# Performance work log

Hardware: AMD Instinct MI355X
Metric: run time of the kernel (lower is better)

Reference implementation:

```python
import jax, jax.numpy as jnp
import numpy as np

N_NODES = 100000
N_EDGES = 3200000
N_GRAPHS = 1024


def gcn_conv(x, src, dst, W, b):
    """GCNConv with symmetric normalization and implicit self-loops.
    x: [N, Fin], src/dst: [E] int, W: [Fin, Fout], b: [Fout]."""
    n = x.shape[0]
    h = x @ W  # [N, Fout]
    # degree including self-loop
    deg = jnp.zeros((n,), h.dtype).at[dst].add(1.0) + 1.0
    dinv = deg ** -0.5
    norm = dinv[src] * dinv[dst]  # [E]
    agg = jnp.zeros_like(h).at[dst].add(norm[:, None] * h[src])
    # self-loop contribution: dinv[i]^2 * h[i]
    agg = agg + (dinv * dinv)[:, None] * h
    return agg + b


def setup_inputs() -> dict:
    key = jax.random.key(0)
    ks = jax.random.split(key, 12)
    F, H = 128, 64
    x = jax.random.normal(ks[0], (N_NODES, F), jnp.float32)
    edge_index = jax.random.randint(ks[1], (2, N_EDGES), 0, N_NODES, jnp.int32)
    batch = jnp.sort(jax.random.randint(ks[2], (N_NODES,), 0, N_GRAPHS, jnp.int32))
    def w(k, i, o):
        return jax.random.normal(k, (i, o), jnp.float32) * (1.0 / np.sqrt(i))
    return {
        "x": x, "edge_index": edge_index, "batch": batch,
        "W1": w(ks[3], F, H), "b1": jnp.zeros((H,), jnp.float32),
        "W2": w(ks[4], H, H), "b2": jnp.zeros((H,), jnp.float32),
        "W3": w(ks[5], H, H // 2), "b3": jnp.zeros((H // 2,), jnp.float32),
        "Wc1": w(ks[6], H // 2, H // 4), "bc1": jnp.zeros((H // 4,), jnp.float32),
        "Wc2": w(ks[7], H // 4, 16), "bc2": jnp.zeros((16,), jnp.float32),
    }


def reference(x, edge_index, batch, W1, b1, W2, b2, W3, b3, Wc1, bc1, Wc2, bc2):
    src, dst = edge_index[0], edge_index[1]
    h = jax.nn.relu(gcn_conv(x, src, dst, W1, b1))
    h = jax.nn.relu(gcn_conv(h, src, dst, W2, b2))
    h = jax.nn.relu(gcn_conv(h, src, dst, W3, b3))
    # global mean pool over graphs (dropout is identity at inference)
    sums = jax.ops.segment_sum(h, batch, num_segments=N_GRAPHS)
    counts = jax.ops.segment_sum(jnp.ones((h.shape[0],), h.dtype), batch,
                                 num_segments=N_GRAPHS)
    pooled = sums / jnp.maximum(counts, 1.0)[:, None]  # [G, 32]
    z = jax.nn.relu(pooled @ Wc1 + bc1)
    logits = z @ Wc2 + bc2
    return jax.nn.log_softmax(logits, axis=-1)
```

## Files before the change

### kernel.cpp

```cpp
#include <hip/hip_runtime.h>
#include <hip/hip_bf16.h>
#include <hip/hip_fp16.h>
#include <math.h>


constexpr int BSHIFT = 8;
constexpr int BMASK  = 255;
constexpr int BCAP   = 10240;
constexpr int EPB    = 4096;

__global__ __launch_bounds__(512) void partition_kernel(const int* __restrict__ src,
    const int* __restrict__ dst, int* __restrict__ bucket_cnt,
    unsigned* __restrict__ part, unsigned* __restrict__ runmap,
    int E, int nbuckets, int nblk) {
  __shared__ int lcnt[512];
  __shared__ int lscan[512];
  __shared__ int lcur[512];
  __shared__ unsigned spay[EPB];
  const int t = threadIdx.x;
  const int blk = blockIdx.x;
  const int base = blk * EPB;
  const int lim = min(EPB, E - base);
  int s[8], d[8];
#pragma unroll
  for (int j = 0; j < 8; ++j) {
    int idx = base + j * 512 + t;
    if (idx < E) { s[j] = src[idx]; d[j] = dst[idx]; } else d[j] = -1;
  }
  lcnt[t] = 0;
  __syncthreads();
#pragma unroll
  for (int j = 0; j < 8; ++j)
    if (d[j] >= 0) atomicAdd(&lcnt[d[j] >> BSHIFT], 1);
  __syncthreads();
  const int myv = lcnt[t];
  lscan[t] = myv;
  __syncthreads();
  for (int dd = 1; dd < 512; dd <<= 1) {
    int v = 0;
    if (t >= dd) v = lscan[t - dd];
    __syncthreads();
    if (t >= dd) lscan[t] += v;
    __syncthreads();
  }
  const int excl = lscan[t] - myv;
  if (t < nbuckets) {
    runmap[(size_t)t * nblk + blk] = (unsigned)excl | ((unsigned)myv << 16);
    if (myv > 0) atomicAdd(&bucket_cnt[t], myv);
  }
  lcur[t] = excl;
  __syncthreads();
#pragma unroll
  for (int j = 0; j < 8; ++j) {
    if (d[j] >= 0) {
      int b = d[j] >> BSHIFT;
      int pos = atomicAdd(&lcur[b], 1);
      spay[pos] = ((unsigned)(d[j] & BMASK) << 17) | (unsigned)s[j];
    }
  }
  __syncthreads();
#pragma unroll
  for (int j = 0; j < 8; ++j) {
    int i = j * 512 + t;
    if (i < lim) part[base + i] = spay[i];
  }
}

__global__ __launch_bounds__(256) void scan_buckets_kernel(const int* __restrict__ cnt,
    int* __restrict__ base, int nb) {
  __shared__ int sh[512];
  const int t = threadIdx.x;
  sh[t] = (t < nb) ? cnt[t] : 0;
  sh[t + 256] = (t + 256 < nb) ? cnt[t + 256] : 0;
  __syncthreads();
  for (int d = 1; d < 512; d <<= 1) {
    int v0 = 0, v1 = 0;
    if (t >= d) v0 = sh[t - d];
    if (t + 256 >= d) v1 = sh[t + 256 - d];
    __syncthreads();
    if (t >= d) sh[t] += v0;
    if (t + 256 >= d) sh[t + 256] += v1;
    __syncthreads();
  }
  if (t < nb) base[t] = (t == 0) ? 0 : sh[t - 1];
  if (t + 256 < nb) base[t + 256] = sh[t + 255];
}

__global__ __launch_bounds__(512) void fill_bucket_kernel(
    const unsigned* __restrict__ part, const unsigned* __restrict__ runmap,
    const int* __restrict__ bucket_cnt, const int* __restrict__ bucket_base,
    int* __restrict__ offs, float* __restrict__ dinv, int* __restrict__ csr,
    int N, int E, int nblk) {
  __shared__ unsigned ebuf[BCAP];
  __shared__ int rsh[1024];
  __shared__ int ldeg[256];
  __shared__ int lscan[512];
  const int b = blockIdx.x;
  const int t = threadIdx.x;
  const int nb0 = b << BSHIFT;
  const int nn = min(1 << BSHIFT, N - nb0);
  const int wbase = bucket_base[b];
  const int cnt = min(bucket_cnt[b], BCAP);
  const unsigned r0 = (t < nblk) ? runmap[(size_t)b * nblk + t] : 0u;
  const unsigned r1 = (t + 512 < nblk) ? runmap[(size_t)b * nblk + t + 512] : 0u;
  const int c0 = (int)(r0 >> 16), c1 = (int)(r1 >> 16);
  rsh[t] = c0; rsh[t + 512] = c1;
  if (t < 256) ldeg[t] = 0;
  __syncthreads();
  for (int dd = 1; dd < 1024; dd <<= 1) {
    int x0 = 0, x1 = 0;
    if (t >= dd) x0 = rsh[t - dd];
    x1 = rsh[t + 512 - dd];
    __syncthreads();
    if (t >= dd) rsh[t] += x0;
    rsh[t + 512] += x1;
    __syncthreads();
  }
  {
    int rb = rsh[t] - c0;
    if (c0 > 0) {
      const unsigned* p = part + (size_t)t * EPB + (r0 & 0xFFFFu);
      for (int k = 0; k < c0; ++k) { int o = rb + k; if (o < BCAP) ebuf[o] = p[k]; }
    }
    int rb1 = rsh[t + 512] - c1;
    if (c1 > 0) {
      const unsigned* p = part + (size_t)(t + 512) * EPB + (r1 & 0xFFFFu);
      for (int k = 0; k < c1; ++k) { int o = rb1 + k; if (o < BCAP) ebuf[o] = p[k]; }
    }
  }
  __syncthreads();
  for (int i = t; i < cnt; i += 512) atomicAdd(&ldeg[ebuf[i] >> 17], 1);
  __syncthreads();
  const int myv = (t < 256) ? ldeg[t] : 0;
  lscan[t] = myv;
  __syncthreads();
  for (int d = 1; d < 256; d <<= 1) {
    int v = 0;
    if (t >= d && t < 256) v = lscan[t - d];
    __syncthreads();
    if (t >= d && t < 256) lscan[t] += v;
    __syncthreads();
  }
  const int excl = lscan[t] - myv;
  if (t < nn) {
    offs[nb0 + t] = wbase + excl;
    dinv[nb0 + t] = rsqrtf((float)(myv + 1));
  }
  if (t == 0 && nb0 + nn == N) offs[N] = E;
  if (t < 256) ldeg[t] = excl;
  __syncthreads();
  for (int i = t; i < cnt; i += 512) {
    unsigned v = ebuf[i];
    int pos = atomicAdd(&ldeg[v >> 17], 1);
    if (pos < BCAP) csr[wbase + pos] = (int)(v & 0x1FFFF);
  }
}

template <int K, int M>
__global__ __launch_bounds__(256) void gemm_kernel(const float* __restrict__ X,
    const float* __restrict__ W, __half* __restrict__ Y, int n) {
  constexpr int RPB = 32;
  constexpr int XST = K + 4;
  constexpr int MC = M / 16;
  __shared__ __align__(16) float Ws[K * M];
  __shared__ __align__(16) float Xs[RPB * XST];
  const int tid = threadIdx.x;
  const int row0 = blockIdx.x * RPB;
  for (int i = tid * 4; i < K * M; i += 1024)
    *reinterpret_cast<float4*>(&Ws[i]) = *reinterpret_cast<const float4*>(&W[i]);
  for (int i = tid * 4; i < RPB * K; i += 1024) {
    int r = i / K, k = i - r * K;
    int gr = row0 + r;
    float4 v = make_float4(0.f, 0.f, 0.f, 0.f);
    if (gr < n) v = *reinterpret_cast<const float4*>(&X[(size_t)gr * K + k]);
    *reinterpret_cast<float4*>(&Xs[r * XST + k]) = v;
  }
  __syncthreads();
  const int rt = tid & 15;
  const int c = tid >> 4;
  float acc[2][MC];
#pragma unroll
  for (int rr = 0; rr < 2; ++rr)
#pragma unroll
    for (int j = 0; j < MC; ++j) acc[rr][j] = 0.f;
  for (int k4 = 0; k4 < K; k4 += 4) {
    float4 xv[2];
#pragma unroll
    for (int rr = 0; rr < 2; ++rr)
      xv[rr] = *reinterpret_cast<const float4*>(&Xs[(rt + 16 * rr) * XST + k4]);
    const float* xf0 = reinterpret_cast<const float*>(&xv[0]);
    const float* xf1 = reinterpret_cast<const float*>(&xv[1]);
#pragma unroll
    for (int kk = 0; kk < 4; ++kk) {
      float w[MC];
#pragma unroll
      for (int j = 0; j < MC; ++j) w[j] = Ws[(k4 + kk) * M + c * MC + j];
      float x0 = xf0[kk], x1 = xf1[kk];
#pragma unroll
      for (int j = 0; j < MC; ++j) {
        acc[0][j] += x0 * w[j];
        acc[1][j] += x1 * w[j];
      }
    }
  }
#pragma unroll
  for (int rr = 0; rr < 2; ++rr) {
    int gr = row0 + rt + 16 * rr;
    if (gr < n) {
#pragma unroll
      for (int j = 0; j < MC; ++j)
        Y[(size_t)gr * M + c * MC + j] = __float2half(acc[rr][j]);
    }
  }
}

__device__ inline void h8_acc(uint4 r, float w, float* acc) {
  const __half2* hp = reinterpret_cast<const __half2*>(&r);
#pragma unroll
  for (int q = 0; q < 4; ++q) {
    float2 f = __half22float2(hp[q]);
    acc[2 * q]     += w * f.x;
    acc[2 * q + 1] += w * f.y;
  }
}

template <int FOUT>
__global__ __launch_bounds__(256) void agg_gemm_kernel(
    const __half* __restrict__ h, const int* __restrict__ offs,
    const int* __restrict__ csr, const float* __restrict__ dinv,
    const float* __restrict__ bias, const float* __restrict__ W,
    __half* __restrict__ y, int n) {
  constexpr int FIN = 64;
  constexpr int XST = FIN + 4;
  __shared__ float Xs[32 * XST];
  __shared__ __align__(16) float Wls[FIN * FOUT];
  const int t = threadIdx.x;
  for (int i = t * 4; i < FIN * FOUT; i += 1024)
    *reinterpret_cast<float4*>(&Wls[i]) = *reinterpret_cast<const float4*>(&W[i]);
  const int r = t >> 3;
  const int node = blockIdx.x * 32 + r;
  const int fl = (t & 7) * 8;
  float acc[8];
#pragma unroll
  for (int j = 0; j < 8; ++j) acc[j] = 0.f;
  if (node < n) {
    const int e0 = offs[node], e1 = offs[node + 1];
    const float di = dinv[node];
    {
      uint4 rr = *reinterpret_cast<const uint4*>(h + (size_t)node * FIN + fl);
      h8_acc(rr, di * di, acc);
    }
    int e = e0;
    for (; e + 4 <= e1; e += 4) {
      int sidx[4];
      float wv[4];
      uint4 rv[4];
#pragma unroll
      for (int u = 0; u < 4; ++u) sidx[u] = csr[e + u];
#pragma unroll
      for (int u = 0; u < 4; ++u) wv[u] = di * dinv[sidx[u]];
#pragma unroll
      for (int u = 0; u < 4; ++u)
        rv[u] = *reinterpret_cast<const uint4*>(h + (size_t)sidx[u] * FIN + fl);
#pragma unroll
      for (int u = 0; u < 4; ++u) h8_acc(rv[u], wv[u], acc);
    }
    for (; e < e1; ++e) {
      int s = csr[e];
      uint4 rr = *reinterpret_cast<const uint4*>(h + (size_t)s * FIN + fl);
      h8_acc(rr, di * dinv[s], acc);
    }
#pragma unroll
    for (int j = 0; j < 8; ++j)
      Xs[r * XST + fl + j] = fmaxf(acc[j] + bias[fl + j], 0.f);
  }
  __syncthreads();
  constexpr int CPT = FOUT / 8;
  const int c0 = (t & 7) * CPT;
  float a2[CPT];
#pragma unroll
  for (int j = 0; j < CPT; ++j) a2[j] = 0.f;
  for (int k = 0; k < FIN; ++k) {
    float xv = Xs[r * XST + k];
    const float4 wa = *reinterpret_cast<const float4*>(&Wls[k * FOUT + c0]);
    a2[0] += xv * wa.x; a2[1] += xv * wa.y;
    a2[2] += xv * wa.z; a2[3] += xv * wa.w;
    if constexpr (CPT == 8) {
      const float4 wb = *reinterpret_cast<const float4*>(&Wls[k * FOUT + c0 + 4]);
      a2[4] += xv * wb.x; a2[5] += xv * wb.y;
      a2[6] += xv * wb.z; a2[7] += xv * wb.w;
    }
  }
  if (node < n) {
    union { __half hh[CPT]; uint4 u4; uint2 u2; } cv;
#pragma unroll
    for (int j = 0; j < CPT; ++j) cv.hh[j] = __float2half(a2[j]);
    if constexpr (CPT == 8)
      *reinterpret_cast<uint4*>(y + (size_t)node * FOUT + c0) = cv.u4;
    else
      *reinterpret_cast<uint2*>(y + (size_t)node * FOUT + c0) = cv.u2;
  }
}

__global__ __launch_bounds__(256) void agg_pool_kernel(const __half* __restrict__ h,
    const int* __restrict__ offs, const int* __restrict__ csr,
    const float* __restrict__ dinv, const float* __restrict__ bias,
    const int* __restrict__ batch, float* __restrict__ gsum, int n, int G) {
  constexpr int F = 32;
  constexpr int GCAP = 8;
  __shared__ float lg[GCAP * F];
  const int t = threadIdx.x;
  const int node0 = blockIdx.x * 64;
  const int node = node0 + (t >> 2);
  const int fl = (t & 3) * 8;
  for (int i = t; i < GCAP * F; i += 256) lg[i] = 0.f;
  __syncthreads();
  const int g0 = batch[node0 < n ? node0 : (n - 1)];
  if (node < n) {
    const int e0 = offs[node], e1 = offs[node + 1];
    const float di = dinv[node];
    float acc[8];
#pragma unroll
    for (int j = 0; j < 8; ++j) acc[j] = 0.f;
    {
      uint4 rr = *reinterpret_cast<const uint4*>(h + (size_t)node * F + fl);
      h8_acc(rr, di * di, acc);
    }
    int e = e0;
    for (; e + 4 <= e1; e += 4) {
      int sidx[4];
      float wv[4];
      uint4 rv[4];
#pragma unroll
      for (int u = 0; u < 4; ++u) sidx[u] = csr[e + u];
#pragma unroll
      for (int u = 0; u < 4; ++u) wv[u] = di * dinv[sidx[u]];
#pragma unroll
      for (int u = 0; u < 4; ++u)
        rv[u] = *reinterpret_cast<const uint4*>(h + (size_t)sidx[u] * F + fl);
#pragma unroll
      for (int u = 0; u < 4; ++u) h8_acc(rv[u], wv[u], acc);
    }
    for (; e < e1; ++e) {
      int s = csr[e];
      uint4 rr = *reinterpret_cast<const uint4*>(h + (size_t)s * F + fl);
      h8_acc(rr, di * dinv[s], acc);
    }
    const int rel = batch[node] - g0;
    if (rel < GCAP) {
#pragma unroll
      for (int j = 0; j < 8; ++j)
        atomicAdd(&lg[rel * F + fl + j], fmaxf(acc[j] + bias[fl + j], 0.f));
    } else {
      float* gp = gsum + (size_t)batch[node] * F + fl;
#pragma unroll
      for (int j = 0; j < 8; ++j)
        atomicAdd(&gp[j], fmaxf(acc[j] + bias[fl + j], 0.f));
    }
  }
  __syncthreads();
  for (int i = t; i < GCAP * F; i += 256) {
    float v = lg[i];
    int gi = g0 * F + i;
    if (v != 0.f && gi < G * F) atomicAdd(&gsum[gi], v);
  }
}

__global__ __launch_bounds__(256) void head_kernel(const float* __restrict__ gsum,
    const int* __restrict__ batch, const float* __restrict__ Wc1,
    const float* __restrict__ bc1, const float* __restrict__ Wc2,
    const float* __restrict__ bc2, float* __restrict__ out, int n, int G) {
  int g = blockIdx.x * blockDim.x + threadIdx.x;
  if (g >= G) return;
  int lo = 0, hi = n;
  while (lo < hi) { int m = (lo + hi) >> 1; if (batch[m] < g) lo = m + 1; else hi = m; }
  const int s0 = lo;
  lo = s0; hi = n;
  while (lo < hi) { int m = (lo + hi) >> 1; if (batch[m] < g + 1) lo = m + 1; else hi = m; }
  const float inv = 1.0f / fmaxf((float)(lo - s0), 1.0f);
  float p[32];
#pragma unroll
  for (int k = 0; k < 32; ++k) p[k] = gsum[g * 32 + k] * inv;
  float z[16];
#pragma unroll
  for (int j = 0; j < 16; ++j) {
    float a = bc1[j];
#pragma unroll
    for (int k = 0; k < 32; ++k) a += p[k] * Wc1[k * 16 + j];
    z[j] = fmaxf(a, 0.f);
  }
  float lg[16];
  float m = -1e30f;
#pragma unroll
  for (int j = 0; j < 16; ++j) {
    float a = bc2[j];
#pragma unroll
    for (int k = 0; k < 16; ++k) a += z[k] * Wc2[k * 16 + j];
    lg[j] = a;
    m = fmaxf(m, a);
  }
  float ssum = 0.f;
#pragma unroll
  for (int j = 0; j < 16; ++j) ssum += expf(lg[j] - m);
  float lse = logf(ssum);
#pragma unroll
  for (int j = 0; j < 16; ++j) out[g * 16 + j] = lg[j] - m - lse;
}

extern "C" void kernel_launch(void* const* d_in, const int* in_sizes, int n_in,
                              void* d_out, int out_size, void* d_ws, size_t ws_size,
                              hipStream_t stream) {
  const float* x   = (const float*)d_in[0];
  const int*   ei  = (const int*)d_in[1];
  const int*   batch = (const int*)d_in[2];
  const float* W1 = (const float*)d_in[3];
  const float* b1 = (const float*)d_in[4];
  const float* W2 = (const float*)d_in[5];
  const float* b2 = (const float*)d_in[6];
  const float* W3 = (const float*)d_in[7];
  const float* b3 = (const float*)d_in[8];
  const float* Wc1 = (const float*)d_in[9];
  const float* bc1 = (const float*)d_in[10];
  const float* Wc2 = (const float*)d_in[11];
  const float* bc2 = (const float*)d_in[12];

  const int N = in_sizes[2];
  const int E = in_sizes[1] / 2;
  const int G = out_size / 16;
  const int* src = ei;
  const int* dst = ei + E;
  const int nbuckets = (N + ((1 << BSHIFT) - 1)) >> BSHIFT;
  const int nblk = (E + EPB - 1) / EPB;

  char* ws = (char*)d_ws;
  size_t off = 0;
  auto alloc = [&](size_t bytes) -> void* {
    void* p = ws + off;
    off += (bytes + 511) & ~(size_t)511;
    return p;
  };
  int*   offs   = (int*)alloc(((size_t)N + 1) * 4);
  float* dinv   = (float*)alloc((size_t)N * 4);
  int*   bucket_cnt  = (int*)alloc(2048);
  int*   bucket_base = (int*)alloc(2048);
  unsigned* runmap = (unsigned*)alloc((size_t)nbuckets * nblk * 4);
  int*   csr    = (int*)alloc((size_t)E * 4);
  __half* hbufA = (__half*)alloc((size_t)N * 64 * 2);
  __half* hbufB = (__half*)alloc((size_t)N * 64 * 2);
  __half* hbufC = (__half*)alloc((size_t)N * 32 * 2);
  float* gsum   = (float*)alloc((size_t)G * 32 * 4);
  unsigned* part = (unsigned*)hbufA;
  (void)ws_size; (void)n_in;

  hipMemsetAsync(bucket_cnt, 0, (size_t)nbuckets * 4, stream);
  hipMemsetAsync(gsum, 0, (size_t)G * 32 * 4, stream);
  partition_kernel<<<nblk, 512, 0, stream>>>(src, dst, bucket_cnt, part, runmap,
                                             E, nbuckets, nblk);
  scan_buckets_kernel<<<1, 256, 0, stream>>>(bucket_cnt, bucket_base, nbuckets);
  fill_bucket_kernel<<<nbuckets, 512, 0, stream>>>(part, runmap, bucket_cnt,
                                                   bucket_base, offs, dinv, csr,
                                                   N, E, nblk);

  gemm_kernel<128, 64><<<(N + 31) / 32, 256, 0, stream>>>(x, W1, hbufA, N);
  agg_gemm_kernel<64><<<(N + 31) / 32, 256, 0, stream>>>(hbufA, offs, csr, dinv,
                                                         b1, W2, hbufB, N);
  agg_gemm_kernel<32><<<(N + 31) / 32, 256, 0, stream>>>(hbufB, offs, csr, dinv,
                                                         b2, W3, hbufC, N);
  agg_pool_kernel<<<(N + 63) / 64, 256, 0, stream>>>(hbufC, offs, csr, dinv,
                                                     b3, batch, gsum, N, G);
  head_kernel<<<(G + 255) / 256, 256, 0, stream>>>(gsum, batch, Wc1, bc1,
                                                   Wc2, bc2, (float*)d_out, N, G);
}
```

Before: 335.7 us.

## Split feature matrices into column halves and gather each half in a separate pass

Intermediate activations are now stored as two contiguous column halves, each N x F/2, instead of one row-major N x F array. The aggregation kernels gather one half at a time across all edges, with twice as many nodes per block and fewer threads per node. The aim is a smaller gather working set per pass for better L2 locality. The cost is that the CSR indices and dinv values are read twice per layer, and there is an extra block-wide sync.

```diff
diff --git a/kernel.cpp b/kernel.cpp
--- a/kernel.cpp
+++ b/kernel.cpp
@@ -162,6 +162,7 @@
   constexpr int RPB = 32;
   constexpr int XST = K + 4;
   constexpr int MC = M / 16;
+  constexpr int HF = M / 2;
   __shared__ __align__(16) float Ws[K * M];
   __shared__ __align__(16) float Xs[RPB * XST];
   const int tid = threadIdx.x;
@@ -203,13 +204,16 @@
       }
     }
   }
+  const int c0 = c * MC;
+  const int oh = c0 / HF, oc = c0 - oh * HF;
 #pragma unroll
   for (int rr = 0; rr < 2; ++rr) {
     int gr = row0 + rt + 16 * rr;
     if (gr < n) {
-#pragma unroll
-      for (int j = 0; j < MC; ++j)
-        Y[(size_t)gr * M + c * MC + j] = __float2half(acc[rr][j]);
+      union { __half hh[MC]; uint2 u2; } cv;
+#pragma unroll
+      for (int j = 0; j < MC; ++j) cv.hh[j] = __float2half(acc[rr][j]);
+      *reinterpret_cast<uint2*>(Y + (size_t)oh * n * HF + (size_t)gr * HF + oc) = cv.u2;
     }
   }
 }
@@ -232,73 +236,80 @@
     __half* __restrict__ y, int n) {
   constexpr int FIN = 64;
   constexpr int XST = FIN + 4;
-  __shared__ float Xs[32 * XST];
+  __shared__ float Xs[64 * XST];
   __shared__ __align__(16) float Wls[FIN * FOUT];
   const int t = threadIdx.x;
   for (int i = t * 4; i < FIN * FOUT; i += 1024)
     *reinterpret_cast<float4*>(&Wls[i]) = *reinterpret_cast<const float4*>(&W[i]);
-  const int r = t >> 3;
-  const int node = blockIdx.x * 32 + r;
-  const int fl = (t & 7) * 8;
-  float acc[8];
-#pragma unroll
-  for (int j = 0; j < 8; ++j) acc[j] = 0.f;
+  const int r = t >> 2;
+  const int node = blockIdx.x * 64 + r;
+  const int fl = (t & 3) * 8;
+  int e0 = 0, e1 = 0;
+  float di = 0.f;
+  if (node < n) { e0 = offs[node]; e1 = offs[node + 1]; di = dinv[node]; }
+  const size_t HS = (size_t)n * 32;
+#pragma unroll
+  for (int half = 0; half < 2; ++half) {
+    const __half* hh = h + (size_t)half * HS + fl;
+    float acc[8];
+#pragma unroll
+    for (int j = 0; j < 8; ++j) acc[j] = 0.f;
+    if (node < n) {
+      {
+        uint4 rr = *reinterpret_cast<const uint4*>(hh + (size_t)node * 32);
+        h8_acc(rr, di * di, acc);
+      }
+      int e = e0;
+      for (; e + 4 <= e1; e += 4) {
+        int sidx[4];
+        float wv[4];
+        uint4 rv[4];
+#pragma unroll
+        for (int u = 0; u < 4; ++u) sidx[u] = csr[e + u];
+#pragma unroll
+        for (int u = 0; u < 4; ++u) wv[u] = di * dinv[sidx[u]];
+#pragma unroll
+        for (int u = 0; u < 4; ++u)
+          rv[u] = *reinterpret_cast<const uint4*>(hh + (size_t)sidx[u] * 32);
+#pragma unroll
+        for (int u = 0; u < 4; ++u) h8_acc(rv[u], wv[u], acc);
+      }
+      for (; e < e1; ++e) {
+        int s = csr[e];
+        uint4 rr = *reinterpret_cast<const uint4*>(hh + (size_t)s * 32);
+        h8_acc(rr, di * dinv[s], acc);
+      }
+      const int fb = half * 32 + fl;
+#pragma unroll
+      for (int j = 0; j < 8; ++j)
+        Xs[r * XST + fb + j] = fmaxf(acc[j] + bias[fb + j], 0.f);
+    }
+    __syncthreads();
+  }
+  constexpr int CPT = FOUT / 4;
+  constexpr int HF = FOUT / 2;
+  const int c0 = (t & 3) * CPT;
+  float o[CPT];
+#pragma unroll
+  for (int j = 0; j < CPT; ++j) o[j] = 0.f;
+  for (int k = 0; k < FIN; ++k) {
+    const float xv = Xs[r * XST + k];
+#pragma unroll
+    for (int j4 = 0; j4 < CPT; j4 += 4) {
+      float4 wv = *reinterpret_cast<const float4*>(&Wls[k * FOUT + c0 + j4]);
+      o[j4] += xv * wv.x; o[j4 + 1] += xv * wv.y;
+      o[j4 + 2] += xv * wv.z; o[j4 + 3] += xv * wv.w;
+    }
+  }
   if (node < n) {
-    const int e0 = offs[node], e1 = offs[node + 1];
-    const float di = dinv[node];
-    {
-      uint4 rr = *reinterpret_cast<const uint4*>(h + (size_t)node * FIN + fl);
-      h8_acc(rr, di * di, acc);
-    }
-    int e = e0;
-    for (; e + 4 <= e1; e += 4) {
-      int sidx[4];
-      float wv[4];
-      uint4 rv[4];
-#pragma unroll
-      for (int u = 0; u < 4; ++u) sidx[u] = csr[e + u];
-#pragma unroll
-      for (int u = 0; u < 4; ++u) wv[u] = di * dinv[sidx[u]];
-#pragma unroll
-      for (int u = 0; u < 4; ++u)
-        rv[u] = *reinterpret_cast<const uint4*>(h + (size_t)sidx[u] * FIN + fl);
-#pragma unroll
-      for (int u = 0; u < 4; ++u) h8_acc(rv[u], wv[u], acc);
-    }
-    for (; e < e1; ++e) {
-      int s = csr[e];
-      uint4 rr = *reinterpret_cast<const uint4*>(h + (size_t)s * FIN + fl);
-      h8_acc(rr, di * dinv[s], acc);
-    }
-#pragma unroll
-    for (int j = 0; j < 8; ++j)
-      Xs[r * XST + fl + j] = fmaxf(acc[j] + bias[fl + j], 0.f);
-  }
-  __syncthreads();
-  constexpr int CPT = FOUT / 8;
-  const int c0 = (t & 7) * CPT;
-  float a2[CPT];
-#pragma unroll
-  for (int j = 0; j < CPT; ++j) a2[j] = 0.f;
-  for (int k = 0; k < FIN; ++k) {
-    float xv = Xs[r * XST + k];
-    const float4 wa = *reinterpret_cast<const float4*>(&Wls[k * FOUT + c0]);
-    a2[0] += xv * wa.x; a2[1] += xv * wa.y;
-    a2[2] += xv * wa.z; a2[3] += xv * wa.w;
-    if constexpr (CPT == 8) {
-      const float4 wb = *reinterpret_cast<const float4*>(&Wls[k * FOUT + c0 + 4]);
-      a2[4] += xv * wb.x; a2[5] += xv * wb.y;
-      a2[6] += xv * wb.z; a2[7] += xv * wb.w;
-    }
-  }
-  if (node < n) {
-    union { __half hh[CPT]; uint4 u4; uint2 u2; } cv;
-#pragma unroll
-    for (int j = 0; j < CPT; ++j) cv.hh[j] = __float2half(a2[j]);
-    if constexpr (CPT == 8)
-      *reinterpret_cast<uint4*>(y + (size_t)node * FOUT + c0) = cv.u4;
-    else
-      *reinterpret_cast<uint2*>(y + (size_t)node * FOUT + c0) = cv.u2;
+    const int oh = c0 / HF, oc = c0 - oh * HF;
+    union { __half hh[CPT]; uint4 u4[CPT / 8]; } cv;
+#pragma unroll
+    for (int j = 0; j < CPT; ++j) cv.hh[j] = __float2half(o[j]);
+    uint4* dst4 = reinterpret_cast<uint4*>(y + (size_t)oh * n * HF +
+                                           (size_t)node * HF + oc);
+#pragma unroll
+    for (int j = 0; j < CPT / 8; ++j) dst4[j] = cv.u4[j];
   }
 }
 
@@ -306,63 +317,72 @@
     const int* __restrict__ offs, const int* __restrict__ csr,
     const float* __restrict__ dinv, const float* __restrict__ bias,
     const int* __restrict__ batch, float* __restrict__ gsum, int n, int G) {
-  constexpr int F = 32;
   constexpr int GCAP = 8;
-  __shared__ float lg[GCAP * F];
+  __shared__ float lg[GCAP * 32];
   const int t = threadIdx.x;
-  const int node0 = blockIdx.x * 64;
-  const int node = node0 + (t >> 2);
-  const int fl = (t & 3) * 8;
-  for (int i = t; i < GCAP * F; i += 256) lg[i] = 0.f;
+  const int node0 = blockIdx.x * 128;
+  const int r = t >> 1;
+  const int node = node0 + r;
+  const int fl = (t & 1) * 8;
+  for (int i = t; i < GCAP * 32; i += 256) lg[i] = 0.f;
   __syncthreads();
   const int g0 = batch[node0 < n ? node0 : (n - 1)];
+  int e0 = 0, e1 = 0, g = -1, rel = 0;
+  float di = 0.f;
   if (node < n) {
-    const int e0 = offs[node], e1 = offs[node + 1];
-    const float di = dinv[node];
+    e0 = offs[node]; e1 = offs[node + 1]; di = dinv[node];
+    g = batch[node]; rel = g - g0;
+  }
+  const size_t HS = (size_t)n * 16;
+#pragma unroll
+  for (int half = 0; half < 2; ++half) {
+    const __half* hh = h + (size_t)half * HS + fl;
     float acc[8];
 #pragma unroll
     for (int j = 0; j < 8; ++j) acc[j] = 0.f;
-    {
-      uint4 rr = *reinterpret_cast<const uint4*>(h + (size_t)node * F + fl);
-      h8_acc(rr, di * di, acc);
-    }
-    int e = e0;
-    for (; e + 4 <= e1; e += 4) {
-      int sidx[4];
-      float wv[4];
-      uint4 rv[4];
-#pragma unroll
-      for (int u = 0; u < 4; ++u) sidx[u] = csr[e + u];
-#pragma unroll
-      for (int u = 0; u < 4; ++u) wv[u] = di * dinv[sidx[u]];
-#pragma unroll
-      for (int u = 0; u < 4; ++u)
-        rv[u] = *reinterpret_cast<const uint4*>(h + (size_t)sidx[u] * F + fl);
-#pragma unroll
-      for (int u = 0; u < 4; ++u) h8_acc(rv[u], wv[u], acc);
-    }
-    for (; e < e1; ++e) {
-      int s = csr[e];
-      uint4 rr = *reinterpret_cast<const uint4*>(h + (size_t)s * F + fl);
-      h8_acc(rr, di * dinv[s], acc);
-    }
-    const int rel = batch[node] - g0;
-    if (rel < GCAP) {
-#pragma unroll
-      for (int j = 0; j < 8; ++j)
-        atomicAdd(&lg[rel * F + fl + j], fmaxf(acc[j] + bias[fl + j], 0.f));
-    } else {
-      float* gp = gsum + (size_t)batch[node] * F + fl;
-#pragma unroll
-      for (int j = 0; j < 8; ++j)
-        atomicAdd(&gp[j], fmaxf(acc[j] + bias[fl + j], 0.f));
-    }
-  }
-  __syncthreads();
-  for (int i = t; i < GCAP * F; i += 256) {
+    if (node < n) {
+      {
+        uint4 rr = *reinterpret_cast<const uint4*>(hh + (size_t)node * 16);
+        h8_acc(rr, di * di, acc);
+      }
+      int e = e0;
+      for (; e + 4 <= e1; e += 4) {
+        int sidx[4];
+        float wv[4];
+        uint4 rv[4];
+#pragma unroll
+        for (int u = 0; u < 4; ++u) sidx[u] = csr[e + u];
+#pragma unroll
+        for (int u = 0; u < 4; ++u) wv[u] = di * dinv[sidx[u]];
+#pragma unroll
+        for (int u = 0; u < 4; ++u)
+          rv[u] = *reinterpret_cast<const uint4*>(hh + (size_t)sidx[u] * 16);
+#pragma unroll
+        for (int u = 0; u < 4; ++u) h8_acc(rv[u], wv[u], acc);
+      }
+      for (; e < e1; ++e) {
+        int s = csr[e];
+        uint4 rr = *reinterpret_cast<const uint4*>(hh + (size_t)s * 16);
+        h8_acc(rr, di * dinv[s], acc);
+      }
+      const int fb = half * 16 + fl;
+      if (rel < GCAP) {
+#pragma unroll
+        for (int j = 0; j < 8; ++j)
+          atomicAdd(&lg[rel * 32 + fb + j], fmaxf(acc[j] + bias[fb + j], 0.f));
+      } else {
+#pragma unroll
+        for (int j = 0; j < 8; ++j)
+          atomicAdd(&gsum[(size_t)g * 32 + fb + j],
+                    fmaxf(acc[j] + bias[fb + j], 0.f));
+      }
+    }
+    __syncthreads();
+  }
+  for (int i = t; i < GCAP * 32; i += 256) {
     float v = lg[i];
-    int gi = g0 * F + i;
-    if (v != 0.f && gi < G * F) atomicAdd(&gsum[gi], v);
+    int gi = g0 * 32 + i;
+    if (v != 0.f && gi < G * 32) atomicAdd(&gsum[gi], v);
   }
 }
 
@@ -462,12 +482,12 @@
                                                    N, E, nblk);
 
   gemm_kernel<128, 64><<<(N + 31) / 32, 256, 0, stream>>>(x, W1, hbufA, N);
-  agg_gemm_kernel<64><<<(N + 31) / 32, 256, 0, stream>>>(hbufA, offs, csr, dinv,
+  agg_gemm_kernel<64><<<(N + 63) / 64, 256, 0, stream>>>(hbufA, offs, csr, dinv,
                                                          b1, W2, hbufB, N);
-  agg_gemm_kernel<32><<<(N + 31) / 32, 256, 0, stream>>>(hbufB, offs, csr, dinv,
+  agg_gemm_kernel<32><<<(N + 63) / 64, 256, 0, stream>>>(hbufB, offs, csr, dinv,
                                                          b2, W3, hbufC, N);
-  agg_pool_kernel<<<(N + 63) / 64, 256, 0, stream>>>(hbufC, offs, csr, dinv,
-                                                     b3, batch, gsum, N, G);
+  agg_pool_kernel<<<(N + 127) / 128, 256, 0, stream>>>(hbufC, offs, csr, dinv,
+                                                       b3, batch, gsum, N, G);
   head_kernel<<<(G + 255) / 256, 256, 0, stream>>>(gsum, batch, Wc1, bc1,
                                                    Wc2, bc2, (float*)d_out, N, G);
 }
```

Result: slower. 475.8 us, median of 2 (+41.7%).
